# Kernel optimization log

Hardware: AMD Instinct MI355X
Metric: run time of the kernel (lower is better)

## Reference

```python
import jax, jax.numpy as jnp
import numpy as np

SCALE_FACTOR = 10.0   # activation_scale_factor
POST_ROOT = 2.0       # post_product_root


def setup_inputs() -> dict:
    key = jax.random.key(0)
    k_x, k_w, k_b = jax.random.split(key, 3)
    N, F = 2097152, 64
    input = jax.random.normal(k_x, (N, F), dtype=jnp.float32)
    # trainable weight init: uniform(-1/sqrt(F), 1/sqrt(F)); avoid exact zeros not needed here
    bound = 1.0 / np.sqrt(F)
    weight = jax.random.uniform(k_w, (F,), dtype=jnp.float32, minval=-bound, maxval=bound)
    bias = jax.random.normal(k_b, (F,), dtype=jnp.float32) * 0.01
    return {"input": input, "weight": weight, "bias": bias}


def reference(input, weight, bias):
    # matmul with diag(weight) is just an elementwise per-feature scale
    targets = input * weight + bias                      # [N, F]
    targets = jax.nn.sigmoid(SCALE_FACTOR * targets)     # [N, F]
    targets = targets ** (1.0 / POST_ROOT)               # [N, F]
    return jnp.prod(targets, axis=1)                     # [N]
```

## Files before the change

kernel.cpp:

```cpp
#include <hip/hip_runtime.h>


typedef float vfloat4 __attribute__((ext_vector_type(4)));

__device__ __forceinline__ float exp2_hw(float x) {
    float r; asm("v_exp_f32 %0, %1" : "=v"(r) : "v"(x)); return r;
}
__device__ __forceinline__ float rsq_hw(float x) {
    float r; asm("v_rsq_f32 %0, %1" : "=v"(r) : "v"(x)); return r;
}

template <int PAT>
__device__ __forceinline__ float bfly_mul(float p) {
    int q = __builtin_amdgcn_ds_swizzle(__builtin_bit_cast(int, p), PAT);
    return p * __builtin_bit_cast(float, q);
}
__device__ __forceinline__ float group16_prod(float p) {
    p = bfly_mul<0x041F>(p);
    p = bfly_mul<0x081F>(p);
    p = bfly_mul<0x101F>(p);
    p = bfly_mul<0x201F>(p);
    return p;
}

__global__ __launch_bounds__(256) void one2one_prod_kernel(
    const vfloat4* __restrict__ in4,
    const float*   __restrict__ w,
    const float*   __restrict__ b,
    float*         __restrict__ out,
    int total_f4)
{
    const float C = -14.4269504088896340736f;
    const int grp = threadIdx.x & 15;

    const vfloat4 wv = ((const vfloat4*)w)[grp];
    const vfloat4 bv = ((const vfloat4*)b)[grp];
    const float a0 = C * wv.x, a1 = C * wv.y, a2 = C * wv.z, a3 = C * wv.w;
    const float d0 = C * bv.x, d1 = C * bv.y, d2 = C * bv.z, d3 = C * bv.w;

    const int stride = gridDim.x * blockDim.x;
    int f = blockIdx.x * blockDim.x + threadIdx.x;

    for (; f + stride < total_f4; f += 2 * stride) {
        vfloat4 x = __builtin_nontemporal_load(&in4[f]);
        vfloat4 y = __builtin_nontemporal_load(&in4[f + stride]);

        float px = (1.0f + exp2_hw(fmaf(x.x, a0, d0)))
                 * (1.0f + exp2_hw(fmaf(x.y, a1, d1)))
                 * (1.0f + exp2_hw(fmaf(x.z, a2, d2)))
                 * (1.0f + exp2_hw(fmaf(x.w, a3, d3)));
        float py = (1.0f + exp2_hw(fmaf(y.x, a0, d0)))
                 * (1.0f + exp2_hw(fmaf(y.y, a1, d1)))
                 * (1.0f + exp2_hw(fmaf(y.z, a2, d2)))
                 * (1.0f + exp2_hw(fmaf(y.w, a3, d3)));

        px = group16_prod(px);
        py = group16_prod(py);

        if (grp == 0) {
            out[f >> 4]            = rsq_hw(px);
            out[(f + stride) >> 4] = rsq_hw(py);
        }
    }
    if (f < total_f4) {
        vfloat4 x = __builtin_nontemporal_load(&in4[f]);
        float px = (1.0f + exp2_hw(fmaf(x.x, a0, d0)))
                 * (1.0f + exp2_hw(fmaf(x.y, a1, d1)))
                 * (1.0f + exp2_hw(fmaf(x.z, a2, d2)))
                 * (1.0f + exp2_hw(fmaf(x.w, a3, d3)));
        px = group16_prod(px);
        if (grp == 0) out[f >> 4] = rsq_hw(px);
    }
}

extern "C" void kernel_launch(void* const* d_in, const int* in_sizes, int n_in,
                              void* d_out, int out_size, void* d_ws, size_t ws_size,
                              hipStream_t stream) {
    const vfloat4* in4 = (const vfloat4*)d_in[0];
    const float*   w   = (const float*)d_in[1];
    const float*   b   = (const float*)d_in[2];
    float* out = (float*)d_out;

    const int total_f4 = in_sizes[0] / 4;

    const int block = 256;
    const int grid  = 8192;
    hipLaunchKernelGGL(one2one_prod_kernel, dim3(grid), dim3(block), 0, stream,
                       in4, w, b, out, total_f4);
}
```

Measured before the change: 668.8 us.

## Unroll grid-stride loop to four rows, drop nontemporal loads, fold products into FMAs

Raises the per-iteration unroll from two to four independent float4 loads so more memory requests are in flight per thread. Switches from nontemporal loads to ordinary loads, and rewrites the running product (1+e) chains as fmaf(p,e,p) to save a few VALU ops. The tail becomes a loop to handle up to three leftover strides. Costs more registers, which may lower occupancy.

After: 685.9 us. 1.03x slower.

```diff
diff --git a/kernel.cpp b/kernel.cpp
--- a/kernel.cpp
+++ b/kernel.cpp
@@ -23,6 +23,20 @@
     return p;
 }
 
+__device__ __forceinline__ float row_partial(vfloat4 x,
+                                             float a0, float a1, float a2, float a3,
+                                             float d0, float d1, float d2, float d3) {
+    float e0 = exp2_hw(fmaf(x.x, a0, d0));
+    float e1 = exp2_hw(fmaf(x.y, a1, d1));
+    float e2 = exp2_hw(fmaf(x.z, a2, d2));
+    float e3 = exp2_hw(fmaf(x.w, a3, d3));
+    float p = 1.0f + e0;
+    p = fmaf(p, e1, p);
+    p = fmaf(p, e2, p);
+    p = fmaf(p, e3, p);
+    return p;
+}
+
 __global__ __launch_bounds__(256) void one2one_prod_kernel(
     const vfloat4* __restrict__ in4,
     const float*   __restrict__ w,
@@ -41,35 +55,34 @@
     const int stride = gridDim.x * blockDim.x;
     int f = blockIdx.x * blockDim.x + threadIdx.x;
 
-    for (; f + stride < total_f4; f += 2 * stride) {
-        vfloat4 x = __builtin_nontemporal_load(&in4[f]);
-        vfloat4 y = __builtin_nontemporal_load(&in4[f + stride]);
+    for (; f + 3 * stride < total_f4; f += 4 * stride) {
+        vfloat4 x0 = in4[f];
+        vfloat4 x1 = in4[f + stride];
+        vfloat4 x2 = in4[f + 2 * stride];
+        vfloat4 x3 = in4[f + 3 * stride];
 
-        float px = (1.0f + exp2_hw(fmaf(x.x, a0, d0)))
-                 * (1.0f + exp2_hw(fmaf(x.y, a1, d1)))
-                 * (1.0f + exp2_hw(fmaf(x.z, a2, d2)))
-                 * (1.0f + exp2_hw(fmaf(x.w, a3, d3)));
-        float py = (1.0f + exp2_hw(fmaf(y.x, a0, d0)))
-                 * (1.0f + exp2_hw(fmaf(y.y, a1, d1)))
-                 * (1.0f + exp2_hw(fmaf(y.z, a2, d2)))
-                 * (1.0f + exp2_hw(fmaf(y.w, a3, d3)));
+        float p0 = row_partial(x0, a0, a1, a2, a3, d0, d1, d2, d3);
+        float p1 = row_partial(x1, a0, a1, a2, a3, d0, d1, d2, d3);
+        float p2 = row_partial(x2, a0, a1, a2, a3, d0, d1, d2, d3);
+        float p3 = row_partial(x3, a0, a1, a2, a3, d0, d1, d2, d3);
 
-        px = group16_prod(px);
-        py = group16_prod(py);
+        p0 = group16_prod(p0);
+        p1 = group16_prod(p1);
+        p2 = group16_prod(p2);
+        p3 = group16_prod(p3);
 
         if (grp == 0) {
-            out[f >> 4]            = rsq_hw(px);
-            out[(f + stride) >> 4] = rsq_hw(py);
+            out[f >> 4]                  = rsq_hw(p0);
+            out[(f + stride) >> 4]       = rsq_hw(p1);
+            out[(f + 2 * stride) >> 4]   = rsq_hw(p2);
+            out[(f + 3 * stride) >> 4]   = rsq_hw(p3);
         }
     }
-    if (f < total_f4) {
-        vfloat4 x = __builtin_nontemporal_load(&in4[f]);
-        float px = (1.0f + exp2_hw(fmaf(x.x, a0, d0)))
-                 * (1.0f + exp2_hw(fmaf(x.y, a1, d1)))
-                 * (1.0f + exp2_hw(fmaf(x.z, a2, d2)))
-                 * (1.0f + exp2_hw(fmaf(x.w, a3, d3)));
-        px = group16_prod(px);
-        if (grp == 0) out[f >> 4] = rsq_hw(px);
+    for (; f < total_f4; f += stride) {
+        vfloat4 x = in4[f];
+        float p = row_partial(x, a0, a1, a2, a3, d0, d1, d2, d3);
+        p = group16_prod(p);
+        if (grp == 0) out[f >> 4] = rsq_hw(p);
     }
 }
 
```
